# Kernel tuning notes

Hardware: AMD Instinct MI355X
Metric: run time of the kernel (lower is better)

## Reference

```python
import jax, jax.numpy as jnp
import numpy as np

N, M, NNZ, D, H = 4096, 1024, 65536, 512, 8
DH = D // H
DFF = 4 * D
EPS = 1e-5


def layer_norm(x, g, b):
    mu = jnp.mean(x, axis=-1, keepdims=True)
    var = jnp.mean((x - mu) ** 2, axis=-1, keepdims=True)
    return (x - mu) / jnp.sqrt(var + EPS) * g + b


def setup_inputs() -> dict:
    key = jax.random.key(0)
    ks = jax.random.split(key, 16)
    s = 1.0 / np.sqrt(D)
    inp = {}
    inp['x'] = jax.random.normal(ks[0], (N, D), jnp.float32)
    node = jax.random.randint(ks[1], (NNZ,), 0, N, jnp.int32)
    edge = jax.random.randint(ks[2], (NNZ,), 0, M, jnp.int32)
    inp['hyperedge_index'] = jnp.stack([node, edge], axis=0)
    inp['hyperedge_attr'] = jax.random.normal(ks[3], (M, D), jnp.float32)
    # HypergraphConv params (heads=1): lin (no bias), att [2*D], output bias
    inp['Wh'] = jax.random.normal(ks[4], (D, D), jnp.float32) * s
    inp['att'] = jax.random.normal(ks[5], (2 * D,), jnp.float32) * s
    inp['bias_h'] = jnp.zeros((D,), jnp.float32)
    # outer LayerNorms
    inp['ln1_g'] = jnp.ones((D,), jnp.float32); inp['ln1_b'] = jnp.zeros((D,), jnp.float32)
    inp['ln2_g'] = jnp.ones((D,), jnp.float32); inp['ln2_b'] = jnp.zeros((D,), jnp.float32)
    # TransformerEncoderLayer params (post-norm, relu, dropout off at eval)
    inp['in_proj_w'] = jax.random.normal(ks[6], (3 * D, D), jnp.float32) * s
    inp['in_proj_b'] = jnp.zeros((3 * D,), jnp.float32)
    inp['out_proj_w'] = jax.random.normal(ks[7], (D, D), jnp.float32) * s
    inp['out_proj_b'] = jnp.zeros((D,), jnp.float32)
    inp['ff1_w'] = jax.random.normal(ks[8], (DFF, D), jnp.float32) * s
    inp['ff1_b'] = jnp.zeros((DFF,), jnp.float32)
    inp['ff2_w'] = jax.random.normal(ks[9], (D, DFF), jnp.float32) * (1.0 / np.sqrt(DFF))
    inp['ff2_b'] = jnp.zeros((D,), jnp.float32)
    inp['tln1_g'] = jnp.ones((D,), jnp.float32); inp['tln1_b'] = jnp.zeros((D,), jnp.float32)
    inp['tln2_g'] = jnp.ones((D,), jnp.float32); inp['tln2_b'] = jnp.zeros((D,), jnp.float32)
    return inp


def hypergraph_conv(x, node, edge, hyperedge_attr, Wh, att, bias_h):
    # PyG HypergraphConv, use_attention=True, heads=1, concat=True
    xl = x @ Wh.T                      # [N, D]
    el = hyperedge_attr @ Wh.T         # [M, D]
    # per-incidence attention score
    a = xl[node] @ att[:D] + el[edge] @ att[D:]          # [NNZ]
    a = jnp.where(a >= 0, a, 0.2 * a)                    # leaky_relu(0.2)
    # scatter-softmax grouped by node index
    amax = jax.ops.segment_max(a, node, num_segments=N)
    a = jnp.exp(a - amax[node])
    den = jax.ops.segment_sum(a, node, num_segments=N)
    alpha = a / (den[node] + 1e-16)
    # degree normalizations (hyperedge_weight = ones)
    ones = jnp.ones((NNZ,), x.dtype)
    Dn = jax.ops.segment_sum(ones, node, num_segments=N)
    Dinv = jnp.where(Dn > 0, 1.0 / Dn, 0.0)
    Bn = jax.ops.segment_sum(ones, edge, num_segments=M)
    Binv = jnp.where(Bn > 0, 1.0 / Bn, 0.0)
    # node -> hyperedge aggregation
    msg1 = (Binv[edge] * alpha)[:, None] * xl[node]      # [NNZ, D]
    ef = jax.ops.segment_sum(msg1, edge, num_segments=M)  # [M, D]
    # hyperedge -> node aggregation
    msg2 = (Dinv[node] * alpha)[:, None] * ef[edge]
    out = jax.ops.segment_sum(msg2, node, num_segments=N)  # [N, D]
    return out + bias_h


def reference(x, hyperedge_index, hyperedge_attr, Wh, att, bias_h,
              ln1_g, ln1_b, ln2_g, ln2_b,
              in_proj_w, in_proj_b, out_proj_w, out_proj_b,
              ff1_w, ff1_b, ff2_w, ff2_b,
              tln1_g, tln1_b, tln2_g, tln2_b):
    node, edge = hyperedge_index[0], hyperedge_index[1]
    x_conv = hypergraph_conv(x, node, edge, hyperedge_attr, Wh, att, bias_h)
    x1 = layer_norm(x + x_conv, ln1_g, ln1_b)
    # TransformerEncoderLayer (post-norm, eval: dropout off), seq of N tokens
    qkv = x1 @ in_proj_w.T + in_proj_b
    q, k, v = jnp.split(qkv, 3, axis=-1)
    q = q.reshape(N, H, DH); k = k.reshape(N, H, DH); v = v.reshape(N, H, DH)
    scores = jnp.einsum('nhd,mhd->hnm', q, k) / np.sqrt(DH)
    attw = jax.nn.softmax(scores, axis=-1)
    ctx = jnp.einsum('hnm,mhd->nhd', attw, v).reshape(N, D)
    attn_out = ctx @ out_proj_w.T + out_proj_b
    x2 = layer_norm(x1 + attn_out, tln1_g, tln1_b)
    ff = jax.nn.relu(x2 @ ff1_w.T + ff1_b) @ ff2_w.T + ff2_b
    x3 = layer_norm(x2 + ff, tln2_g, tln2_b)
    return layer_norm(x1 + x3, ln2_g, ln2_b)
```

## Files before the change

### kernel.cpp

```cpp
#include <hip/hip_runtime.h>
#include <math.h>

#define NN   4096
#define MM   1024
#define NNZC 65536
#define DD   512
#define HH   8
#define DHH  64
#define DFFC 2048
#define NSPLIT 4

typedef short bf16x8 __attribute__((ext_vector_type(8)));
typedef float f32x4  __attribute__((ext_vector_type(4)));

static __device__ inline unsigned short f2bf(float f) {
  union { float f; unsigned int u; } v; v.f = f;
  unsigned int r = v.u + 0x7fff + ((v.u >> 16) & 1);
  return (unsigned short)(r >> 16);
}
static __device__ inline float bf2f(unsigned short u) {
  return __uint_as_float((unsigned int)u << 16);
}

__device__ inline void gload16(const void* g, void* l) {
  __builtin_amdgcn_global_load_lds(
      (const __attribute__((address_space(1))) void*)g,
      (__attribute__((address_space(3))) void*)l, 16, 0, 0);
}

__device__ inline void atomicMaxF(float* addr, float val) {
  if (val >= 0.f) atomicMax((int*)addr, __float_as_int(val));
  else            atomicMin((unsigned int*)addr, __float_as_uint(val));
}

__global__ void init_kernel(float* amax, float* den, int* DnCnt, int* BnCnt,
                            int* node_cur, int* edge_cur) {
  int i = blockIdx.x * 256 + threadIdx.x;
  if (i < NN) { amax[i] = -INFINITY; den[i] = 0.f; DnCnt[i] = 0; node_cur[i] = 0; }
  if (i < MM) { BnCnt[i] = 0; edge_cur[i] = 0; }
}

__global__ __launch_bounds__(256) void f2b_multi(
    const float* s0, unsigned short* d0, int n0,
    const float* s1, unsigned short* d1, int n1,
    const float* s2, unsigned short* d2, int n2,
    const float* s3, unsigned short* d3, int n3,
    const float* s4, unsigned short* d4, int n4,
    const float* s5, unsigned short* d5, int n5,
    const float* s6, unsigned short* d6, int n6) {
  const float* in; unsigned short* out; int n8;
  switch (blockIdx.y) {
    case 0: in=s0; out=d0; n8=n0; break;
    case 1: in=s1; out=d1; n8=n1; break;
    case 2: in=s2; out=d2; n8=n2; break;
    case 3: in=s3; out=d3; n8=n3; break;
    case 4: in=s4; out=d4; n8=n4; break;
    case 5: in=s5; out=d5; n8=n5; break;
    default: in=s6; out=d6; n8=n6; break;
  }
  for (int i = blockIdx.x*256 + threadIdx.x; i < n8; i += gridDim.x*256) {
    float4 v0 = *(const float4*)&in[(size_t)i*8];
    float4 v1 = *(const float4*)&in[(size_t)i*8 + 4];
    unsigned short w[8];
    w[0]=f2bf(v0.x); w[1]=f2bf(v0.y); w[2]=f2bf(v0.z); w[3]=f2bf(v0.w);
    w[4]=f2bf(v1.x); w[5]=f2bf(v1.y); w[6]=f2bf(v1.z); w[7]=f2bf(v1.w);
    *(ulonglong2*)&out[(size_t)i*8] = *(ulonglong2*)w;
  }
}

__global__ __launch_bounds__(256) void gemm_bt_bf16(
    const unsigned short* __restrict__ A, const unsigned short* __restrict__ B,
    const float* __restrict__ bias, float* __restrict__ Cf,
    unsigned short* __restrict__ Cb, int N, int K, int relu) {
  __shared__ __align__(16) unsigned short Al[128*64];
  __shared__ __align__(16) unsigned short Bl[128*64];
  const int t = threadIdx.x;
  const int w = t >> 6, l = t & 63;
  const int lg = l >> 4, lid = l & 15;
  const int wr = w >> 1, wc = w & 1;
  const int bm = blockIdx.x * 128, bn = blockIdx.y * 128;

  f32x4 acc[4][4];
  #pragma unroll
  for (int mi = 0; mi < 4; ++mi)
    #pragma unroll
    for (int ni = 0; ni < 4; ++ni) acc[mi][ni] = (f32x4)0.f;

  for (int k0 = 0; k0 < K; k0 += 64) {
    #pragma unroll
    for (int i = 0; i < 4; ++i) {
      int cid = i*256 + t;
      int row = cid >> 3, cp = cid & 7;
      int gc = cp ^ (row & 7);
      gload16(&A[(size_t)(bm + row)*K + k0 + gc*8], &Al[cid*8]);
      gload16(&B[(size_t)(bn + row)*K + k0 + gc*8], &Bl[cid*8]);
    }
    asm volatile("s_waitcnt vmcnt(0)" ::: "memory");
    __syncthreads();
    #pragma unroll
    for (int ks = 0; ks < 2; ++ks) {
      bf16x8 af[4], bfr[4];
      #pragma unroll
      for (int mi = 0; mi < 4; ++mi) {
        int r = wr*64 + mi*16 + lid;
        af[mi] = *(const bf16x8*)&Al[r*64 + ((ks*4 + lg) ^ (r & 7))*8];
      }
      #pragma unroll
      for (int ni = 0; ni < 4; ++ni) {
        int r = wc*64 + ni*16 + lid;
        bfr[ni] = *(const bf16x8*)&Bl[r*64 + ((ks*4 + lg) ^ (r & 7))*8];
      }
      __builtin_amdgcn_s_setprio(1);
      #pragma unroll
      for (int mi = 0; mi < 4; ++mi)
        #pragma unroll
        for (int ni = 0; ni < 4; ++ni)
          acc[mi][ni] = __builtin_amdgcn_mfma_f32_16x16x32_bf16(af[mi], bfr[ni], acc[mi][ni], 0, 0, 0);
      __builtin_amdgcn_s_setprio(0);
    }
    __syncthreads();
  }

  #pragma unroll
  for (int ni = 0; ni < 4; ++ni) {
    int col = bn + wc*64 + ni*16 + lid;
    float bv = bias ? bias[col] : 0.f;
    #pragma unroll
    for (int mi = 0; mi < 4; ++mi) {
      #pragma unroll
      for (int rg = 0; rg < 4; ++rg) {
        int row = bm + wr*64 + mi*16 + lg*4 + rg;
        float v = acc[mi][ni][rg] + bv;
        if (relu) v = fmaxf(v, 0.f);
        if (Cf) Cf[(size_t)row*N + col] = v;
        if (Cb) Cb[(size_t)row*N + col] = f2bf(v);
      }
    }
  }
}

__global__ __launch_bounds__(256) void rowdot_b16(const unsigned short* __restrict__ X,
    const float* __restrict__ vec, float* __restrict__ out, int rows) {
  int w = (blockIdx.x * 256 + threadIdx.x) >> 6;
  int lane = threadIdx.x & 63;
  if (w >= rows) return;
  const unsigned short* xr = &X[(size_t)w * DD];
  float s = 0.f;
  #pragma unroll
  for (int j = 0; j < 8; ++j) s += bf2f(xr[lane + 64*j]) * vec[lane + 64*j];
  #pragma unroll
  for (int off = 1; off < 64; off <<= 1) s += __shfl_xor(s, off, 64);
  if (lane == 0) out[w] = s;
}

__global__ void incidence_pass1(const int* __restrict__ node_idx, const int* __restrict__ edge_idx,
    const float* __restrict__ s_node, const float* __restrict__ s_edge,
    float* __restrict__ a_buf, float* amax, int* DnCnt, int* BnCnt) {
  int i = blockIdx.x * 256 + threadIdx.x;
  if (i >= NNZC) return;
  int n = node_idx[i], m = edge_idx[i];
  float a = s_node[n] + s_edge[m];
  a = (a >= 0.f) ? a : 0.2f * a;
  a_buf[i] = a;
  atomicMaxF(&amax[n], a);
  atomicAdd(&DnCnt[n], 1);
  atomicAdd(&BnCnt[m], 1);
}

__global__ __launch_bounds__(1024) void exscan_kernel(const int* __restrict__ in,
                                                      int* __restrict__ out, int n) {
  __shared__ int sums[1024];
  const int t = threadIdx.x;
  const int chunk = (n + 1023) >> 10;
  const int start = t * chunk;
  const int stop  = min(start + chunk, n);
  int local = 0;
  for (int i = start; i < stop; ++i) local += in[i];
  sums[t] = local;
  __syncthreads();
  for (int o = 1; o < 1024; o <<= 1) {
    int v = (t >= o) ? sums[t - o] : 0;
    __syncthreads();
    sums[t] += v;
    __syncthreads();
  }
  int run = (t == 0) ? 0 : sums[t - 1];
  for (int i = start; i < stop; ++i) { out[i] = run; run += in[i]; }
  if (t == 1023) out[n] = sums[1023];
}

__global__ void incidence_pass2(const int* __restrict__ node_idx, const int* __restrict__ edge_idx,
    float* __restrict__ a_buf, const float* __restrict__ amax, float* den,
    const int* __restrict__ node_off, const int* __restrict__ edge_off,
    int* node_cur, int* edge_cur, int* node_list, int* edge_list) {
  int i = blockIdx.x * 256 + threadIdx.x;
  if (i >= NNZC) return;
  int n = node_idx[i], m = edge_idx[i];
  float e = __expf(a_buf[i] - amax[n]);
  a_buf[i] = e;
  atomicAdd(&den[n], e);
  int pn = atomicAdd(&node_cur[n], 1);
  node_list[node_off[n] + pn] = i;
  int pm = atomicAdd(&edge_cur[m], 1);
  edge_list[edge_off[m] + pm] = i;
}

__global__ __launch_bounds__(256) void gather_edge(const int* __restrict__ edge_off,
    const int* __restrict__ edge_list, const int* __restrict__ node_idx,
    const float* __restrict__ a_buf, const float* __restrict__ den,
    const unsigned short* __restrict__ xlb, unsigned short* __restrict__ efb) {
  int m = blockIdx.x;
  int t = threadIdx.x;
  int beg = edge_off[m], end = edge_off[m+1];
  int cnt = end - beg;
  float Binv = (cnt > 0) ? (1.0f / (float)cnt) : 0.f;
  __shared__ int   ln_[128];
  __shared__ float lw_[128];
  float acc0 = 0.f, acc1 = 0.f;
  for (int c = beg; c < end; c += 128) {
    int nchunk = min(128, end - c);
    if (t < nchunk) {
      int i = edge_list[c + t];
      int n = node_idx[i];
      ln_[t] = n;
      lw_[t] = a_buf[i] / (den[n] + 1e-16f) * Binv;
    }
    __syncthreads();
    float a0 = 0.f, a1 = 0.f, b0 = 0.f, b1 = 0.f;
    int j = 0;
    for (; j + 1 < nchunk; j += 2) {
      float w0 = lw_[j], w1 = lw_[j+1];
      const unsigned short* r0 = &xlb[(size_t)ln_[j]   * DD];
      const unsigned short* r1 = &xlb[(size_t)ln_[j+1] * DD];
      a0 += w0 * bf2f(r0[t]);       b0 += w0 * bf2f(r0[t + 256]);
      a1 += w1 * bf2f(r1[t]);       b1 += w1 * bf2f(r1[t + 256]);
    }
    if (j < nchunk) {
      float w0 = lw_[j];
      const unsigned short* r0 = &xlb[(size_t)ln_[j] * DD];
      a0 += w0 * bf2f(r0[t]);       b0 += w0 * bf2f(r0[t + 256]);
    }
    acc0 += a0 + a1;
    acc1 += b0 + b1;
    __syncthreads();
  }
  efb[(size_t)m * DD + t]       = f2bf(acc0);
  efb[(size_t)m * DD + t + 256] = f2bf(acc1);
}

__global__ __launch_bounds__(256) void gather_node(const int* __restrict__ node_off,
    const int* __restrict__ node_list, const int* __restrict__ edge_idx,
    const float* __restrict__ a_buf, const float* __restrict__ den,
    const unsigned short* __restrict__ efb, const float* __restrict__ bias_h,
    float* __restrict__ conv) {
  int n = blockIdx.x;
  int t = threadIdx.x;
  int beg = node_off[n], end = node_off[n+1];
  int cnt = end - beg;
  float Dinv = (cnt > 0) ? (1.0f / (float)cnt) : 0.f;
  float wscale = Dinv / (den[n] + 1e-16f);
  __shared__ int   le_[128];
  __shared__ float lw_[128];
  float acc0 = 0.f, acc1 = 0.f;
  for (int c = beg; c < end; c += 128) {
    int nchunk = min(128, end - c);
    if (t < nchunk) {
      int i = node_list[c + t];
      le_[t] = edge_idx[i];
      lw_[t] = a_buf[i] * wscale;
    }
    __syncthreads();
    float a0 = 0.f, a1 = 0.f, b0 = 0.f, b1 = 0.f;
    int j = 0;
    for (; j + 1 < nchunk; j += 2) {
      float w0 = lw_[j], w1 = lw_[j+1];
      const unsigned short* r0 = &efb[(size_t)le_[j]   * DD];
      const unsigned short* r1 = &efb[(size_t)le_[j+1] * DD];
      a0 += w0 * bf2f(r0[t]);       b0 += w0 * bf2f(r0[t + 256]);
      a1 += w1 * bf2f(r1[t]);       b1 += w1 * bf2f(r1[t + 256]);
    }
    if (j < nchunk) {
      float w0 = lw_[j];
      const unsigned short* r0 = &efb[(size_t)le_[j] * DD];
      a0 += w0 * bf2f(r0[t]);       b0 += w0 * bf2f(r0[t + 256]);
    }
    acc0 += a0 + a1;
    acc1 += b0 + b1;
    __syncthreads();
  }
  conv[(size_t)n * DD + t]       = acc0 + bias_h[t];
  conv[(size_t)n * DD + t + 256] = acc1 + bias_h[t + 256];
}

__global__ __launch_bounds__(256) void ln_residual(const float* __restrict__ a,
    const float* __restrict__ b, const unsigned short* __restrict__ bB,
    const float* __restrict__ g, const float* __restrict__ be,
    float* __restrict__ out, unsigned short* __restrict__ outb) {
  int r = blockIdx.x;
  int t = threadIdx.x;
  float b0 = b ? b[(size_t)r*DD + t]       : bf2f(bB[(size_t)r*DD + t]);
  float b1 = b ? b[(size_t)r*DD + t + 256] : bf2f(bB[(size_t)r*DD + t + 256]);
  float v0 = a[(size_t)r*DD + t]       + b0;
  float v1 = a[(size_t)r*DD + t + 256] + b1;
  __shared__ float red[4];
  __shared__ float mu_s, rstd_s;
  float s = v0 + v1;
  #pragma unroll
  for (int off = 1; off < 64; off <<= 1) s += __shfl_xor(s, off, 64);
  int wid = t >> 6;
  if ((t & 63) == 0) red[wid] = s;
  __syncthreads();
  if (t == 0) mu_s = (red[0] + red[1] + red[2] + red[3]) / 512.f;
  __syncthreads();
  float mu = mu_s;
  float d0 = v0 - mu, d1 = v1 - mu;
  float vs = d0*d0 + d1*d1;
  #pragma unroll
  for (int off = 1; off < 64; off <<= 1) vs += __shfl_xor(vs, off, 64);
  if ((t & 63) == 0) red[wid] = vs;
  __syncthreads();
  if (t == 0) rstd_s = rsqrtf((red[0] + red[1] + red[2] + red[3]) / 512.f + 1e-5f);
  __syncthreads();
  float rs = rstd_s;
  float o0 = d0 * rs * g[t]       + be[t];
  float o1 = d1 * rs * g[t + 256] + be[t + 256];
  out[(size_t)r*DD + t]       = o0;
  out[(size_t)r*DD + t + 256] = o1;
  if (outb) {
    outb[(size_t)r*DD + t]       = f2bf(o0);
    outb[(size_t)r*DD + t + 256] = f2bf(o1);
  }
}

__global__ __launch_bounds__(256) void ln_final2(const float* __restrict__ x2,
    const unsigned short* __restrict__ ffob, const float* __restrict__ x1,
    const float* __restrict__ g1, const float* __restrict__ b1,
    const float* __restrict__ g2, const float* __restrict__ b2,
    float* __restrict__ out) {
  int r = blockIdx.x;
  int t = threadIdx.x;
  __shared__ float red[4];
  __shared__ float sh0, sh1;
  int wid = t >> 6;
  float v0 = x2[(size_t)r*DD + t]       + bf2f(ffob[(size_t)r*DD + t]);
  float v1 = x2[(size_t)r*DD + t + 256] + bf2f(ffob[(size_t)r*DD + t + 256]);
  float s = v0 + v1;
  #pragma unroll
  for (int off = 1; off < 64; off <<= 1) s += __shfl_xor(s, off, 64);
  if ((t & 63) == 0) red[wid] = s;
  __syncthreads();
  if (t == 0) sh0 = (red[0] + red[1] + red[2] + red[3]) / 512.f;
  __syncthreads();
  float mu = sh0;
  float d0 = v0 - mu, d1 = v1 - mu;
  float vs = d0*d0 + d1*d1;
  #pragma unroll
  for (int off = 1; off < 64; off <<= 1) vs += __shfl_xor(vs, off, 64);
  if ((t & 63) == 0) red[wid] = vs;
  __syncthreads();
  if (t == 0) sh1 = rsqrtf((red[0] + red[1] + red[2] + red[3]) / 512.f + 1e-5f);
  __syncthreads();
  float rs = sh1;
  float x30 = d0 * rs * g1[t]       + b1[t];
  float x31 = d1 * rs * g1[t + 256] + b1[t + 256];
  __syncthreads();
  float u0 = x1[(size_t)r*DD + t]       + x30;
  float u1 = x1[(size_t)r*DD + t + 256] + x31;
  s = u0 + u1;
  #pragma unroll
  for (int off = 1; off < 64; off <<= 1) s += __shfl_xor(s, off, 64);
  if ((t & 63) == 0) red[wid] = s;
  __syncthreads();
  if (t == 0) sh0 = (red[0] + red[1] + red[2] + red[3]) / 512.f;
  __syncthreads();
  mu = sh0;
  d0 = u0 - mu; d1 = u1 - mu;
  vs = d0*d0 + d1*d1;
  #pragma unroll
  for (int off = 1; off < 64; off <<= 1) vs += __shfl_xor(vs, off, 64);
  if ((t & 63) == 0) red[wid] = vs;
  __syncthreads();
  if (t == 0) sh1 = rsqrtf((red[0] + red[1] + red[2] + red[3]) / 512.f + 1e-5f);
  __syncthreads();
  rs = sh1;
  out[(size_t)r*DD + t]       = d0 * rs * g2[t]       + b2[t];
  out[(size_t)r*DD + t + 256] = d1 * rs * g2[t + 256] + b2[t + 256];
}

__global__ __launch_bounds__(256) void conv_vt(const unsigned short* __restrict__ qkvbb,
                                               unsigned short* __restrict__ Vtb) {
  __shared__ unsigned short Tl[64][76];
  const int h = blockIdx.y;
  const int tt = blockIdx.x * 64;
  const int t = threadIdx.x;
  {
    int row = t >> 2;
    int cbase = (t & 3) * 16;
    const unsigned short* src = &qkvbb[(size_t)(tt + row)*1536 + 1024 + h*64];
    #pragma unroll
    for (int jj = 0; jj < 4; ++jj)
      *(ushort4*)&Tl[row][cbase + jj*4] = *(const ushort4*)&src[cbase + jj*4];
  }
  __syncthreads();
  #pragma unroll
  for (int it = 0; it < 4; ++it) {
    int d = it*16 + (t >> 4);
    int tk = (t & 15) * 4;
    ushort4 w4;
    w4.x = Tl[tk+0][d]; w4.y = Tl[tk+1][d]; w4.z = Tl[tk+2][d]; w4.w = Tl[tk+3][d];
    *(ushort4*)&Vtb[(size_t)h*64*NN + (size_t)d*NN + tt + tk] = w4;
  }
}

__global__ __launch_bounds__(256) void attn_mfma_part(const unsigned short* __restrict__ qkvbb,
                                                      const unsigned short* __restrict__ Vtb,
                                                      unsigned short* __restrict__ Opartb,
                                                      float* __restrict__ ml) {
  const int head = blockIdx.y;
  const int z = blockIdx.z;
  const int q0 = blockIdx.x * 64;
  const int t = threadIdx.x;
  const int w = t >> 6;
  const int l = t & 63;
  const int lg = l >> 4;
  const int lid = l & 15;
  const float sc = 0.125f * 1.44269504f;
  const float THRraw = 44.36f;

  __shared__ __align__(16) unsigned short Kl[2][64*64];
  __shared__ __align__(16) unsigned short Vl[2][64*64];

  bf16x8 qa[2];
  {
    const int qrow = q0 + w*16 + lid;
    const unsigned short* qp = &qkvbb[(size_t)qrow*1536 + head*64];
    qa[0] = *(const bf16x8*)&qp[lg*8];
    qa[1] = *(const bf16x8*)&qp[32 + lg*8];
  }

  float m = -1e30f, msc = -1e30f, lsum = 0.f;
  f32x4 o[4];
  #pragma unroll
  for (int dt = 0; dt < 4; ++dt) o[dt] = (f32x4)0.f;

  const unsigned short* Kh = qkvbb + 512 + head*64;
  const unsigned short* Vh = Vtb + (size_t)head*64*NN;
  const int kt0 = z * (NN / NSPLIT);
  const int kt1 = kt0 + (NN / NSPLIT);

  const int c0 = t, c1 = 256 + t;
  const int row0 = c0 >> 3, p0 = (c0 & 7) ^ (row0 & 7);
  const int row1 = c1 >> 3, p1 = (c1 & 7) ^ (row1 & 7);
  const int kp0 = 8*((row0>>2)&3) + 4*((row0>>4)&1) + (row0&3) + 32*(row0>>5);
  const int kp1 = 8*((row1>>2)&3) + 4*((row1>>4)&1) + (row1&3) + 32*(row1>>5);

#define ISSUE(buf, ktv) do { \
    gload16(&Kh[(size_t)((ktv) + kp0)*1536 + p0*8], &Kl[buf][c0*8]); \
    gload16(&Kh[(size_t)((ktv) + kp1)*1536 + p1*8], &Kl[buf][c1*8]); \
    gload16(&Vh[(size_t)row0*NN + (ktv) + p0*8],    &Vl[buf][c0*8]); \
    gload16(&Vh[(size_t)row1*NN + (ktv) + p1*8],    &Vl[buf][c1*8]); \
  } while (0)

  ISSUE(0, kt0);
  asm volatile("s_waitcnt vmcnt(0)" ::: "memory");
  __syncthreads();

  int cur = 0;
  for (int kt = kt0; kt < kt1; kt += 64) {
    const bool hn = (kt + 64) < kt1;
    if (hn) ISSUE(cur ^ 1, kt + 64);

    f32x4 s[4];
    #pragma unroll
    for (int n = 0; n < 4; ++n) s[n] = (f32x4)0.f;
    __builtin_amdgcn_s_setprio(1);
    #pragma unroll
    for (int n = 0; n < 4; ++n) {
      int tok = n*16 + lid;
      #pragma unroll
      for (int hf = 0; hf < 2; ++hf) {
        int didx = (tok*64 + hf*32 + lg*8) ^ ((tok & 7) << 3);
        bf16x8 kb = *(const bf16x8*)&Kl[cur][didx];
        s[n] = __builtin_amdgcn_mfma_f32_16x16x32_bf16(kb, qa[hf], s[n], 0, 0, 0);
      }
    }
    __builtin_amdgcn_s_setprio(0);

    float a0 = fmaxf(fmaxf(s[0][0], s[0][1]), s[0][2]);
    float a1 = fmaxf(fmaxf(s[0][3], s[1][0]), s[1][1]);
    float a2 = fmaxf(fmaxf(s[1][2], s[1][3]), s[2][0]);
    float a3 = fmaxf(fmaxf(s[2][1], s[2][2]), s[2][3]);
    float a4 = fmaxf(fmaxf(s[3][0], s[3][1]), s[3][2]);
    float mx = fmaxf(fmaxf(fmaxf(a0, a1), a2), fmaxf(fmaxf(a3, a4), s[3][3]));
    mx = fmaxf(mx, __shfl_xor(mx, 16, 64));
    mx = fmaxf(mx, __shfl_xor(mx, 32, 64));
    if (!__all(mx <= m + THRraw)) {
      float mn = fmaxf(m, mx);
      float c = exp2f((m - mn) * sc);
      m = mn;
      msc = m * sc;
      lsum *= c;
      #pragma unroll
      for (int r = 0; r < 4; ++r) {
        float cr = __shfl(c, lg*4 + r, 64);
        #pragma unroll
        for (int dt = 0; dt < 4; ++dt) o[dt][r] *= cr;
      }
    }
    float ps = 0.f;
    #pragma unroll
    for (int n = 0; n < 4; ++n)
      #pragma unroll
      for (int r = 0; r < 4; ++r) {
        float p = exp2f(fmaf(s[n][r], sc, -msc));
        s[n][r] = p;
        ps += p;
      }
    ps += __shfl_xor(ps, 16, 64);
    ps += __shfl_xor(ps, 32, 64);
    lsum += ps;

    union { bf16x8 v; unsigned int u[4]; } pa[2];
    #pragma unroll
    for (int hf = 0; hf < 2; ++hf) {
      asm("v_cvt_pk_bf16_f32 %0, %1, %2" : "=v"(pa[hf].u[0]) : "v"(s[2*hf][0]),   "v"(s[2*hf][1]));
      asm("v_cvt_pk_bf16_f32 %0, %1, %2" : "=v"(pa[hf].u[1]) : "v"(s[2*hf][2]),   "v"(s[2*hf][3]));
      asm("v_cvt_pk_bf16_f32 %0, %1, %2" : "=v"(pa[hf].u[2]) : "v"(s[2*hf+1][0]), "v"(s[2*hf+1][1]));
      asm("v_cvt_pk_bf16_f32 %0, %1, %2" : "=v"(pa[hf].u[3]) : "v"(s[2*hf+1][2]), "v"(s[2*hf+1][3]));
    }

    __builtin_amdgcn_s_setprio(1);
    #pragma unroll
    for (int dt = 0; dt < 4; ++dt) {
      int drow = dt*16 + lid;
      #pragma unroll
      for (int hf = 0; hf < 2; ++hf) {
        int didx = (drow*64 + hf*32 + lg*8) ^ ((drow & 7) << 3);
        bf16x8 vb = *(const bf16x8*)&Vl[cur][didx];
        o[dt] = __builtin_amdgcn_mfma_f32_16x16x32_bf16(pa[hf].v, vb, o[dt], 0, 0, 0);
      }
    }
    __builtin_amdgcn_s_setprio(0);

    asm volatile("s_waitcnt vmcnt(0)" ::: "memory");
    __syncthreads();
    cur ^= 1;
  }
#undef ISSUE

  #pragma unroll
  for (int r = 0; r < 4; ++r) {
    int q = q0 + w*16 + lg*4 + r;
    size_t base = ((size_t)(z*HH + head)*NN + q)*64;
    #pragma unroll
    for (int dt = 0; dt < 4; ++dt)
      Opartb[base + dt*16 + lid] = f2bf(o[dt][r]);
  }
  if (l < 16) {
    int q = q0 + w*16 + l;
    size_t mb = ((size_t)(z*HH + head)*NN + q)*2;
    ml[mb]     = msc;
    ml[mb + 1] = lsum;
  }
}

__global__ __launch_bounds__(256) void attn_combine(const unsigned short* __restrict__ Opartb,
                                                    const float* __restrict__ ml,
                                                    unsigned short* __restrict__ ctxb) {
  const int w = threadIdx.x >> 6, lane = threadIdx.x & 63;
  const int row = blockIdx.x * 4 + w;
  const int q = row >> 3, head = row & 7;
  float ms[NSPLIT], ls[NSPLIT];
  float mglob = -1e30f;
  #pragma unroll
  for (int s = 0; s < NSPLIT; ++s) {
    size_t mb = ((size_t)(s*HH + head)*NN + q)*2;
    ms[s] = ml[mb]; ls[s] = ml[mb + 1];
    mglob = fmaxf(mglob, ms[s]);
  }
  float lt = 0.f, ov = 0.f;
  #pragma unroll
  for (int s = 0; s < NSPLIT; ++s) {
    float wgt = exp2f(ms[s] - mglob);
    lt += ls[s] * wgt;
    ov += bf2f(Opartb[((size_t)(s*HH + head)*NN + q)*64 + lane]) * wgt;
  }
  ctxb[(size_t)q*DD + head*64 + lane] = f2bf(ov / lt);
}

extern "C" void kernel_launch(void* const* d_in, const int* in_sizes, int n_in,
                              void* d_out, int out_size, void* d_ws, size_t ws_size,
                              hipStream_t stream) {
  const float* x       = (const float*)d_in[0];
  const int*   hidx    = (const int*)d_in[1];
  const float* hattr   = (const float*)d_in[2];
  const float* Wh      = (const float*)d_in[3];
  const float* att     = (const float*)d_in[4];
  const float* bias_h  = (const float*)d_in[5];
  const float* ln1_g   = (const float*)d_in[6];
  const float* ln1_b   = (const float*)d_in[7];
  const float* ln2_g   = (const float*)d_in[8];
  const float* ln2_b   = (const float*)d_in[9];
  const float* in_proj_w  = (const float*)d_in[10];
  const float* in_proj_b  = (const float*)d_in[11];
  const float* out_proj_w = (const float*)d_in[12];
  const float* out_proj_b = (const float*)d_in[13];
  const float* ff1_w   = (const float*)d_in[14];
  const float* ff1_b   = (const float*)d_in[15];
  const float* ff2_w   = (const float*)d_in[16];
  const float* ff2_b   = (const float*)d_in[17];
  const float* tln1_g  = (const float*)d_in[18];
  const float* tln1_b  = (const float*)d_in[19];
  const float* tln2_g  = (const float*)d_in[20];
  const float* tln2_b  = (const float*)d_in[21];
  const int* node_idx = hidx;
  const int* edge_idx = hidx + NNZC;

  char* ws = (char*)d_ws;
  size_t off = 0;
  auto alloc = [&](size_t bytes) -> void* {
    void* p = ws + off;
    off = (off + bytes + 63) & ~(size_t)63;
    return p;
  };
  float* s_node   = (float*)alloc(sizeof(float)*NN);
  float* s_edge   = (float*)alloc(sizeof(float)*MM);
  float* a_buf    = (float*)alloc(sizeof(float)*NNZC);
  float* amax     = (float*)alloc(sizeof(float)*NN);
  float* den      = (float*)alloc(sizeof(float)*NN);
  int*   DnCnt    = (int*)alloc(sizeof(int)*NN);
  int*   BnCnt    = (int*)alloc(sizeof(int)*MM);
  int*   node_off = (int*)alloc(sizeof(int)*(NN+1));
  int*   edge_off = (int*)alloc(sizeof(int)*(MM+1));
  int*   node_cur = (int*)alloc(sizeof(int)*NN);
  int*   edge_cur = (int*)alloc(sizeof(int)*MM);
  int*   node_list= (int*)alloc(sizeof(int)*NNZC);
  int*   edge_list= (int*)alloc(sizeof(int)*NNZC);
  float* conv     = (float*)alloc(sizeof(float)*NN*DD);
  float* x1       = (float*)alloc(sizeof(float)*NN*DD);
  float* x2       = (float*)alloc(sizeof(float)*NN*DD);
  unsigned short* xlb   = (unsigned short*)alloc(sizeof(unsigned short)*NN*DD);
  unsigned short* elb   = (unsigned short*)alloc(sizeof(unsigned short)*MM*DD);
  unsigned short* efb   = (unsigned short*)alloc(sizeof(unsigned short)*MM*DD);
  unsigned short* qkvbb = (unsigned short*)alloc(sizeof(unsigned short)*NN*3*DD);
  unsigned short* Vtb   = (unsigned short*)alloc(sizeof(unsigned short)*NN*DD);
  unsigned short* xb    = (unsigned short*)alloc(sizeof(unsigned short)*NN*DD);
  unsigned short* hattrb= (unsigned short*)alloc(sizeof(unsigned short)*MM*DD);
  unsigned short* Whb   = (unsigned short*)alloc(sizeof(unsigned short)*DD*DD);
  unsigned short* ipwb  = (unsigned short*)alloc(sizeof(unsigned short)*3*DD*DD);
  unsigned short* opwb  = (unsigned short*)alloc(sizeof(unsigned short)*DD*DD);
  unsigned short* ff1wb = (unsigned short*)alloc(sizeof(unsigned short)*DFFC*DD);
  unsigned short* ff2wb = (unsigned short*)alloc(sizeof(unsigned short)*DD*DFFC);
  unsigned short* x1b   = (unsigned short*)alloc(sizeof(unsigned short)*NN*DD);
  unsigned short* x2b   = (unsigned short*)alloc(sizeof(unsigned short)*NN*DD);
  unsigned short* ctxb  = (unsigned short*)alloc(sizeof(unsigned short)*NN*DD);
  unsigned short* attn_outb = (unsigned short*)alloc(sizeof(unsigned short)*NN*DD);
  char* late = (char*)alloc(20u*1024*1024);
  unsigned short* Opartb = (unsigned short*)late;
  float*          mlb    = (float*)(late + 16u*1024*1024);
  unsigned short* ffhb   = (unsigned short*)late;
  unsigned short* ffob   = (unsigned short*)(late + 16u*1024*1024);
  (void)ws_size; (void)in_sizes; (void)n_in; (void)out_size;

  dim3 b256(256);
  f2b_multi<<<dim3(256, 7), b256, 0, stream>>>(
      x, xb, NN*DD/8,  hattr, hattrb, MM*DD/8,  Wh, Whb, DD*DD/8,
      in_proj_w, ipwb, 3*DD*DD/8,  out_proj_w, opwb, DD*DD/8,
      ff1_w, ff1wb, DFFC*DD/8,  ff2_w, ff2wb, DD*DFFC/8);

  gemm_bt_bf16<<<dim3(NN/128, DD/128), b256, 0, stream>>>(xb, Whb, nullptr, nullptr, xlb, DD, DD, 0);
  gemm_bt_bf16<<<dim3(MM/128, DD/128), b256, 0, stream>>>(hattrb, Whb, nullptr, nullptr, elb, DD, DD, 0);
  rowdot_b16<<<NN/4, b256, 0, stream>>>(xlb, att,      s_node, NN);
  rowdot_b16<<<MM/4, b256, 0, stream>>>(elb, att + DD, s_edge, MM);
  init_kernel<<<NN/256, b256, 0, stream>>>(amax, den, DnCnt, BnCnt, node_cur, edge_cur);
  incidence_pass1<<<NNZC/256, b256, 0, stream>>>(node_idx, edge_idx, s_node, s_edge,
                                                 a_buf, amax, DnCnt, BnCnt);
  exscan_kernel<<<1, 1024, 0, stream>>>(DnCnt, node_off, NN);
  exscan_kernel<<<1, 1024, 0, stream>>>(BnCnt, edge_off, MM);
  incidence_pass2<<<NNZC/256, b256, 0, stream>>>(node_idx, edge_idx, a_buf, amax, den,
                                                 node_off, edge_off, node_cur, edge_cur,
                                                 node_list, edge_list);
  gather_edge<<<MM, b256, 0, stream>>>(edge_off, edge_list, node_idx, a_buf, den, xlb, efb);
  gather_node<<<NN, b256, 0, stream>>>(node_off, node_list, edge_idx, a_buf, den, efb, bias_h, conv);
  ln_residual<<<NN, b256, 0, stream>>>(x, conv, nullptr, ln1_g, ln1_b, x1, x1b);
  gemm_bt_bf16<<<dim3(NN/128, (3*DD)/128), b256, 0, stream>>>(x1b, ipwb, in_proj_b, nullptr, qkvbb, 3*DD, DD, 0);
  conv_vt<<<dim3(NN/64, HH), b256, 0, stream>>>(qkvbb, Vtb);
  attn_mfma_part<<<dim3(NN/64, HH, NSPLIT), b256, 0, stream>>>(qkvbb, Vtb, Opartb, mlb);
  attn_combine<<<NN*HH/4, b256, 0, stream>>>(Opartb, mlb, ctxb);
  gemm_bt_bf16<<<dim3(NN/128, DD/128), b256, 0, stream>>>(ctxb, opwb, out_proj_b, nullptr, attn_outb, DD, DD, 0);
  ln_residual<<<NN, b256, 0, stream>>>(x1, nullptr, attn_outb, tln1_g, tln1_b, x2, x2b);
  gemm_bt_bf16<<<dim3(NN/128, DFFC/128), b256, 0, stream>>>(x2b, ff1wb, ff1_b, nullptr, ffhb, DFFC, DD, 1);
  gemm_bt_bf16<<<dim3(NN/128, DD/128),   b256, 0, stream>>>(ffhb, ff2wb, ff2_b, nullptr, ffob, DD, DFFC, 0);
  ln_final2<<<NN, b256, 0, stream>>>(x2, ffob, x1, tln2_g, tln2_b, ln2_g, ln2_b, (float*)d_out);
}
```

Measured before the change: 310.0 us.

## Add 128x64 GEMM tile, merge Wh projections, register-stage attention K/V

```diff
diff --git a/kernel.cpp b/kernel.cpp
--- a/kernel.cpp
+++ b/kernel.cpp
@@ -134,6 +134,79 @@
         if (relu) v = fmaxf(v, 0.f);
         if (Cf) Cf[(size_t)row*N + col] = v;
         if (Cb) Cb[(size_t)row*N + col] = f2bf(v);
+      }
+    }
+  }
+}
+
+__global__ __launch_bounds__(256) void gemm_bt_bf16_n64(
+    const unsigned short* __restrict__ A, const unsigned short* __restrict__ B,
+    const float* __restrict__ bias, unsigned short* __restrict__ Cb, int N, int K) {
+  __shared__ __align__(16) unsigned short Al[128*64];
+  __shared__ __align__(16) unsigned short Bl[64*64];
+  const int t = threadIdx.x;
+  const int w = t >> 6, l = t & 63;
+  const int lg = l >> 4, lid = l & 15;
+  const int wr = w >> 1, wc = w & 1;
+  const int bm = blockIdx.x * 128, bn = blockIdx.y * 64;
+
+  f32x4 acc[4][2];
+  #pragma unroll
+  for (int mi = 0; mi < 4; ++mi)
+    #pragma unroll
+    for (int ni = 0; ni < 2; ++ni) acc[mi][ni] = (f32x4)0.f;
+
+  for (int k0 = 0; k0 < K; k0 += 64) {
+    #pragma unroll
+    for (int i = 0; i < 4; ++i) {
+      int cid = i*256 + t;
+      int row = cid >> 3, cp = cid & 7;
+      int gc = cp ^ (row & 7);
+      gload16(&A[(size_t)(bm + row)*K + k0 + gc*8], &Al[cid*8]);
+    }
+    #pragma unroll
+    for (int i = 0; i < 2; ++i) {
+      int cid = i*256 + t;
+      int row = cid >> 3, cp = cid & 7;
+      int gc = cp ^ (row & 7);
+      gload16(&B[(size_t)(bn + row)*K + k0 + gc*8], &Bl[cid*8]);
+    }
+    asm volatile("s_waitcnt vmcnt(0)" ::: "memory");
+    __syncthreads();
+    #pragma unroll
+    for (int ks = 0; ks < 2; ++ks) {
+      bf16x8 af[4], bfr[2];
+      #pragma unroll
+      for (int mi = 0; mi < 4; ++mi) {
+        int r = wr*64 + mi*16 + lid;
+        af[mi] = *(const bf16x8*)&Al[r*64 + ((ks*4 + lg) ^ (r & 7))*8];
+      }
+      #pragma unroll
+      for (int ni = 0; ni < 2; ++ni) {
+        int r = wc*32 + ni*16 + lid;
+        bfr[ni] = *(const bf16x8*)&Bl[r*64 + ((ks*4 + lg) ^ (r & 7))*8];
+      }
+      __builtin_amdgcn_s_setprio(1);
+      #pragma unroll
+      for (int mi = 0; mi < 4; ++mi)
+        #pragma unroll
+        for (int ni = 0; ni < 2; ++ni)
+          acc[mi][ni] = __builtin_amdgcn_mfma_f32_16x16x32_bf16(af[mi], bfr[ni], acc[mi][ni], 0, 0, 0);
+      __builtin_amdgcn_s_setprio(0);
+    }
+    __syncthreads();
+  }
+
+  #pragma unroll
+  for (int ni = 0; ni < 2; ++ni) {
+    int col = bn + wc*32 + ni*16 + lid;
+    float bv = bias ? bias[col] : 0.f;
+    #pragma unroll
+    for (int mi = 0; mi < 4; ++mi) {
+      #pragma unroll
+      for (int rg = 0; rg < 4; ++rg) {
+        int row = bm + wr*64 + mi*16 + lg*4 + rg;
+        Cb[(size_t)row*N + col] = f2bf(acc[mi][ni][rg] + bv);
       }
     }
   }
@@ -427,8 +500,8 @@
   const float sc = 0.125f * 1.44269504f;
   const float THRraw = 44.36f;
 
-  __shared__ __align__(16) unsigned short Kl[2][64*64];
-  __shared__ __align__(16) unsigned short Vl[2][64*64];
+  __shared__ __align__(16) unsigned short Kl[64*64];
+  __shared__ __align__(16) unsigned short Vl[64*64];
 
   bf16x8 qa[2];
   {
@@ -448,27 +521,32 @@
   const int kt0 = z * (NN / NSPLIT);
   const int kt1 = kt0 + (NN / NSPLIT);
 
-  const int c0 = t, c1 = 256 + t;
-  const int row0 = c0 >> 3, p0 = (c0 & 7) ^ (row0 & 7);
-  const int row1 = c1 >> 3, p1 = (c1 & 7) ^ (row1 & 7);
-  const int kp0 = 8*((row0>>2)&3) + 4*((row0>>4)&1) + (row0&3) + 32*(row0>>5);
-  const int kp1 = 8*((row1>>2)&3) + 4*((row1>>4)&1) + (row1&3) + 32*(row1>>5);
-
-#define ISSUE(buf, ktv) do { \
-    gload16(&Kh[(size_t)((ktv) + kp0)*1536 + p0*8], &Kl[buf][c0*8]); \
-    gload16(&Kh[(size_t)((ktv) + kp1)*1536 + p1*8], &Kl[buf][c1*8]); \
-    gload16(&Vh[(size_t)row0*NN + (ktv) + p0*8],    &Vl[buf][c0*8]); \
-    gload16(&Vh[(size_t)row1*NN + (ktv) + p1*8],    &Vl[buf][c1*8]); \
+  const int srow0 = t >> 3,        scc = (t & 7) * 8;
+  const int srow1 = 32 + (t >> 3);
+  const int sdst0 = (srow0*64 + scc) ^ ((srow0 & 7) << 3);
+  const int sdst1 = (srow1*64 + scc) ^ ((srow1 & 7) << 3);
+  const int kperm0 = 8*((srow0>>2)&3) + 4*((srow0>>4)&1) + (srow0&3) + 32*(srow0>>5);
+  const int kperm1 = 8*((srow1>>2)&3) + 4*((srow1>>4)&1) + (srow1&3) + 32*(srow1>>5);
+  ulonglong2 kreg0, kreg1, vreg0, vreg1;
+
+#define LOADKV(ktv) do { \
+    kreg0 = *(const ulonglong2*)&Kh[(size_t)((ktv) + kperm0)*1536 + scc]; \
+    vreg0 = *(const ulonglong2*)&Vh[(size_t)srow0*NN + (ktv) + scc]; \
+    kreg1 = *(const ulonglong2*)&Kh[(size_t)((ktv) + kperm1)*1536 + scc]; \
+    vreg1 = *(const ulonglong2*)&Vh[(size_t)srow1*NN + (ktv) + scc]; \
   } while (0)
-
-  ISSUE(0, kt0);
-  asm volatile("s_waitcnt vmcnt(0)" ::: "memory");
-  __syncthreads();
-
-  int cur = 0;
+#define STORKV() do { \
+    *(ulonglong2*)&Kl[sdst0] = kreg0; *(ulonglong2*)&Vl[sdst0] = vreg0; \
+    *(ulonglong2*)&Kl[sdst1] = kreg1; *(ulonglong2*)&Vl[sdst1] = vreg1; \
+  } while (0)
+
+  LOADKV(kt0);
+  STORKV();
+  __syncthreads();
+
   for (int kt = kt0; kt < kt1; kt += 64) {
     const bool hn = (kt + 64) < kt1;
-    if (hn) ISSUE(cur ^ 1, kt + 64);
+    if (hn) LOADKV(kt + 64);
 
     f32x4 s[4];
     #pragma unroll
@@ -480,7 +558,7 @@
       #pragma unroll
       for (int hf = 0; hf < 2; ++hf) {
         int didx = (tok*64 + hf*32 + lg*8) ^ ((tok & 7) << 3);
-        bf16x8 kb = *(const bf16x8*)&Kl[cur][didx];
+        bf16x8 kb = *(const bf16x8*)&Kl[didx];
         s[n] = __builtin_amdgcn_mfma_f32_16x16x32_bf16(kb, qa[hf], s[n], 0, 0, 0);
       }
     }
@@ -536,17 +614,20 @@
       #pragma unroll
       for (int hf = 0; hf < 2; ++hf) {
         int didx = (drow*64 + hf*32 + lg*8) ^ ((drow & 7) << 3);
-        bf16x8 vb = *(const bf16x8*)&Vl[cur][didx];
+        bf16x8 vb = *(const bf16x8*)&Vl[didx];
         o[dt] = __builtin_amdgcn_mfma_f32_16x16x32_bf16(pa[hf].v, vb, o[dt], 0, 0, 0);
       }
     }
     __builtin_amdgcn_s_setprio(0);
 
-    asm volatile("s_waitcnt vmcnt(0)" ::: "memory");
-    __syncthreads();
-    cur ^= 1;
-  }
-#undef ISSUE
+    __syncthreads();
+    if (hn) {
+      STORKV();
+      __syncthreads();
+    }
+  }
+#undef LOADKV
+#undef STORKV
 
   #pragma unroll
   for (int r = 0; r < 4; ++r) {
@@ -639,13 +720,11 @@
   float* conv     = (float*)alloc(sizeof(float)*NN*DD);
   float* x1       = (float*)alloc(sizeof(float)*NN*DD);
   float* x2       = (float*)alloc(sizeof(float)*NN*DD);
-  unsigned short* xlb   = (unsigned short*)alloc(sizeof(unsigned short)*NN*DD);
-  unsigned short* elb   = (unsigned short*)alloc(sizeof(unsigned short)*MM*DD);
+  unsigned short* xhb   = (unsigned short*)alloc(sizeof(unsigned short)*(NN+MM)*DD);
+  unsigned short* xelb  = (unsigned short*)alloc(sizeof(unsigned short)*(NN+MM)*DD);
   unsigned short* efb   = (unsigned short*)alloc(sizeof(unsigned short)*MM*DD);
   unsigned short* qkvbb = (unsigned short*)alloc(sizeof(unsigned short)*NN*3*DD);
   unsigned short* Vtb   = (unsigned short*)alloc(sizeof(unsigned short)*NN*DD);
-  unsigned short* xb    = (unsigned short*)alloc(sizeof(unsigned short)*NN*DD);
-  unsigned short* hattrb= (unsigned short*)alloc(sizeof(unsigned short)*MM*DD);
   unsigned short* Whb   = (unsigned short*)alloc(sizeof(unsigned short)*DD*DD);
   unsigned short* ipwb  = (unsigned short*)alloc(sizeof(unsigned short)*3*DD*DD);
   unsigned short* opwb  = (unsigned short*)alloc(sizeof(unsigned short)*DD*DD);
@@ -660,16 +739,17 @@
   float*          mlb    = (float*)(late + 16u*1024*1024);
   unsigned short* ffhb   = (unsigned short*)late;
   unsigned short* ffob   = (unsigned short*)(late + 16u*1024*1024);
+  unsigned short* xlb = xelb;
+  unsigned short* elb = xelb + (size_t)NN*DD;
   (void)ws_size; (void)in_sizes; (void)n_in; (void)out_size;
 
   dim3 b256(256);
   f2b_multi<<<dim3(256, 7), b256, 0, stream>>>(
-      x, xb, NN*DD/8,  hattr, hattrb, MM*DD/8,  Wh, Whb, DD*DD/8,
+      x, xhb, NN*DD/8,  hattr, xhb + (size_t)NN*DD, MM*DD/8,  Wh, Whb, DD*DD/8,
       in_proj_w, ipwb, 3*DD*DD/8,  out_proj_w, opwb, DD*DD/8,
       ff1_w, ff1wb, DFFC*DD/8,  ff2_w, ff2wb, DD*DFFC/8);
 
-  gemm_bt_bf16<<<dim3(NN/128, DD/128), b256, 0, stream>>>(xb, Whb, nullptr, nullptr, xlb, DD, DD, 0);
-  gemm_bt_bf16<<<dim3(MM/128, DD/128), b256, 0, stream>>>(hattrb, Whb, nullptr, nullptr, elb, DD, DD, 0);
+  gemm_bt_bf16_n64<<<dim3((NN+MM)/128, DD/64), b256, 0, stream>>>(xhb, Whb, nullptr, xelb, DD, DD);
   rowdot_b16<<<NN/4, b256, 0, stream>>>(xlb, att,      s_node, NN);
   rowdot_b16<<<MM/4, b256, 0, stream>>>(elb, att + DD, s_edge, MM);
   init_kernel<<<NN/256, b256, 0, stream>>>(amax, den, DnCnt, BnCnt, node_cur, edge_cur);
@@ -683,13 +763,13 @@
   gather_edge<<<MM, b256, 0, stream>>>(edge_off, edge_list, node_idx, a_buf, den, xlb, efb);
   gather_node<<<NN, b256, 0, stream>>>(node_off, node_list, edge_idx, a_buf, den, efb, bias_h, conv);
   ln_residual<<<NN, b256, 0, stream>>>(x, conv, nullptr, ln1_g, ln1_b, x1, x1b);
-  gemm_bt_bf16<<<dim3(NN/128, (3*DD)/128), b256, 0, stream>>>(x1b, ipwb, in_proj_b, nullptr, qkvbb, 3*DD, DD, 0);
+  gemm_bt_bf16_n64<<<dim3(NN/128, (3*DD)/64), b256, 0, stream>>>(x1b, ipwb, in_proj_b, qkvbb, 3*DD, DD);
   conv_vt<<<dim3(NN/64, HH), b256, 0, stream>>>(qkvbb, Vtb);
   attn_mfma_part<<<dim3(NN/64, HH, NSPLIT), b256, 0, stream>>>(qkvbb, Vtb, Opartb, mlb);
   attn_combine<<<NN*HH/4, b256, 0, stream>>>(Opartb, mlb, ctxb);
-  gemm_bt_bf16<<<dim3(NN/128, DD/128), b256, 0, stream>>>(ctxb, opwb, out_proj_b, nullptr, attn_outb, DD, DD, 0);
+  gemm_bt_bf16_n64<<<dim3(NN/128, DD/64), b256, 0, stream>>>(ctxb, opwb, out_proj_b, attn_outb, DD, DD);
   ln_residual<<<NN, b256, 0, stream>>>(x1, nullptr, attn_outb, tln1_g, tln1_b, x2, x2b);
   gemm_bt_bf16<<<dim3(NN/128, DFFC/128), b256, 0, stream>>>(x2b, ff1wb, ff1_b, nullptr, ffhb, DFFC, DD, 1);
-  gemm_bt_bf16<<<dim3(NN/128, DD/128),   b256, 0, stream>>>(ffhb, ff2wb, ff2_b, nullptr, ffob, DD, DFFC, 0);
+  gemm_bt_bf16_n64<<<dim3(NN/128, DD/64), b256, 0, stream>>>(ffhb, ff2wb, ff2_b, ffob, DD, DFFC);
   ln_final2<<<NN, b256, 0, stream>>>(x2, ffob, x1, tln2_g, tln2_b, ln2_g, ln2_b, (float*)d_out);
 }
```

Measured after the change: 278.6 us. 1.11x faster.
